# Kernel tuning notes

Measured on AMD Instinct MI355X. Metric: run time of the kernel, lower is better.

Reference implementation:

```python
import jax, jax.numpy as jnp
import numpy as np

EPS = 1e-10
TEMP = 0.01
THETA = 0.1
BETA = 1.0
GAMMA = 1.0  # FocalLoss(gamma=1)
N, C = 32768, 1000


def setup_inputs() -> dict:
    key = jax.random.key(0)
    k1, k2, k3 = jax.random.split(key, 3)
    probs = jax.random.uniform(k1, (N, C), dtype=jnp.float32)
    probs = probs / jnp.sum(probs, axis=1, keepdims=True)  # valid distributions
    lbl = jax.random.randint(k2, (N,), 0, C)
    y = jax.nn.one_hot(lbl, C, dtype=jnp.float32)
    weights = jax.random.uniform(k3, (N, C), dtype=jnp.float32)
    return {"probs": probs, "y": y, "weights": weights}


def _entropy(p):
    return -jnp.sum(p * jnp.log(jnp.clip(p, EPS)), axis=1)


def _soft_T(e):
    num = e * (1.0 - THETA)
    den = jnp.clip((1.0 - e) * THETA, EPS)
    v = (1.0 / TEMP) * jnp.log(jnp.clip(num / den, EPS))
    return jax.nn.sigmoid(v)


def reference(probs, y, weights):
    num_classes = probs.shape[1]
    entmax = jnp.log(jnp.float32(num_classes))

    predictions = jnp.argmax(probs, axis=1)          # [N]
    labels = jnp.argmax(y)                            # scalar (faithful to original)
    unc = _entropy(probs)                             # [N]

    th_list = jnp.linspace(0.0, 1.0, 21, dtype=jnp.float32)
    umin, umax = jnp.min(unc), jnp.max(unc)
    unc_th = umin + th_list * (umax - umin)           # [21]

    acc = (predictions == labels)                     # [N] bool
    s = _soft_T(unc / entmax)                         # [N]
    t = jnp.tanh(unc)                                 # [N]
    cert_w = (1.0 - s) * (1.0 - t)                    # certain weight
    uncw = s * t                                      # uncertain weight

    le = unc[None, :] <= unc_th[:, None]              # [21, N]
    accb = acc[None, :]
    zero = jnp.float32(0.0)
    n_ac = jnp.sum(jnp.where(le & accb, cert_w[None, :], zero), axis=1)
    n_au = jnp.sum(jnp.where((~le) & accb, uncw[None, :], zero), axis=1)
    n_ic = jnp.sum(jnp.where(le & (~accb), cert_w[None, :], zero), axis=1)
    n_iu = jnp.sum(jnp.where((~le) & (~accb), uncw[None, :], zero), axis=1)

    avu = (n_ac + n_iu) / (n_ac + n_au + n_ic + n_iu + EPS)  # [21]
    # trapezoid rule over th_list (increasing -> direction = 1)
    dx = jnp.diff(th_list)
    auc_avu = jnp.sum(0.5 * (avu[1:] + avu[:-1]) * dx)

    logp = jnp.log(jnp.clip(probs, 1e-08))            # FocalLoss eps = 1e-8
    base = y * logp
    focal_loss = jnp.mean(-jnp.sum(base * weights * (1.0 - probs) ** GAMMA, axis=1))
    ce_loss = jnp.mean(-jnp.sum(base, axis=1))

    savu_loss = -BETA * jnp.log(jnp.clip(auc_avu, EPS)) + focal_loss
    return (savu_loss, ce_loss)
```

## Files before the change

kernel.cpp:

```cpp
#include <hip/hip_runtime.h>
#include <hip/hip_bf16.h>

constexpr int kN = 32768;
constexpr int kC = 1000;
constexpr int NB_A = 2048;
constexpr int NB_B = 1024;
constexpr int NB3 = 512;

__global__ __launch_bounds__(256) void k1_main(
    const float* __restrict__ probs, const float* __restrict__ y,
    const float* __restrict__ wts, float* __restrict__ unc,
    int* __restrict__ pred, float* __restrict__ partMM ,
    float* __restrict__ partCF ) {
  const int lane = threadIdx.x & 63;
  const int wid = threadIdx.x >> 6;

  if (blockIdx.x < NB_A) {
    const int gw = blockIdx.x * 4 + wid;
    float mn = 3.4e38f, mx = -3.4e38f;
#pragma unroll 1
    for (int r = 0; r < 4; ++r) {
      const int i = gw + r * 8192;
      const float* pr = probs + (size_t)i * kC;
      float4 p4[4];
#pragma unroll
      for (int k = 0; k < 4; ++k) {
        const int c0 = k * 256 + lane * 4;
        if (c0 < kC) p4[k] = *reinterpret_cast<const float4*>(pr + c0);
        else p4[k] = make_float4(0.f, 0.f, 0.f, 0.f);
      }
      float ent = 0.f, bv = -3.4e38f; int bi = 0;
#pragma unroll
      for (int k = 0; k < 4; ++k) {
        const int c0 = k * 256 + lane * 4;
#pragma unroll
        for (int j = 0; j < 4; ++j) {
          const float p = (&p4[k].x)[j];
          ent += p * logf(fmaxf(p, 1e-10f));
          if (p > bv) { bv = p; bi = c0 + j; }
        }
      }
#pragma unroll
      for (int off = 32; off; off >>= 1) {
        ent += __shfl_xor(ent, off);
        const float bv2 = __shfl_xor(bv, off);
        const int bi2 = __shfl_xor(bi, off);
        if (bv2 > bv || (bv2 == bv && bi2 < bi)) { bv = bv2; bi = bi2; }
      }
      const float u = -ent;
      if (lane == 0) { unc[i] = u; pred[i] = bi; }
      mn = fminf(mn, u); mx = fmaxf(mx, u);
    }
    __shared__ float sMin[4], sMax[4];
    if (lane == 0) { sMin[wid] = mn; sMax[wid] = mx; }
    __syncthreads();
    if (threadIdx.x == 0) {
      float a = 3.4e38f, b = -3.4e38f;
#pragma unroll
      for (int q = 0; q < 4; ++q) { a = fminf(a, sMin[q]); b = fmaxf(b, sMax[q]); }
      partMM[blockIdx.x * 2 + 0] = a;
      partMM[blockIdx.x * 2 + 1] = b;
    }
  } else {
    const int gwb = (blockIdx.x - NB_A) * 4 + wid;
    constexpr float kLogClip8 = -18.420680743952367f;
    float ce = 0.f, fo = 0.f;
#pragma unroll 1
    for (int r = 0; r < 8; ++r) {
      const int i = gwb + r * 4096;
      const float* yr = y + (size_t)i * kC;
      int lbl = -1;
#pragma unroll 1
      for (int step = 0; step < 4; ++step) {
        const int c0 = step * 256 + lane * 4;
        float4 y4 = make_float4(0.f, 0.f, 0.f, 0.f);
        if (c0 < kC) y4 = *reinterpret_cast<const float4*>(yr + c0);
        int loc = -1;
#pragma unroll
        for (int j = 0; j < 4; ++j) if ((&y4.x)[j] != 0.0f) loc = j;
        if (__any(loc >= 0)) {
          if (loc >= 0) lbl = c0 + loc;
          break;
        }
      }
      if (lbl >= 0) {
        const float p = probs[(size_t)i * kC + lbl];
        const float w = wts[(size_t)i * kC + lbl];
        const float lp = fmaxf(logf(fmaxf(p, 1e-10f)), kLogClip8);
        ce += lp;
        fo += lp * w * (1.0f - p);
      }
    }
#pragma unroll
    for (int off = 32; off; off >>= 1) {
      ce += __shfl_xor(ce, off);
      fo += __shfl_xor(fo, off);
    }
    __shared__ float sCe[4], sFo[4];
    if (lane == 0) { sCe[wid] = ce; sFo[wid] = fo; }
    __syncthreads();
    if (threadIdx.x == 0) {
      float c = 0.f, f = 0.f;
#pragma unroll
      for (int q = 0; q < 4; ++q) { c += sCe[q]; f += sFo[q]; }
      const int bb = blockIdx.x - NB_A;
      partCF[bb * 2 + 0] = c;
      partCF[bb * 2 + 1] = f;
    }
  }
}

__global__ __launch_bounds__(256) void k2_scalars(
    const float* __restrict__ y, const float* __restrict__ partMM,
    const float* __restrict__ partCF, float* __restrict__ scal) {
  const int t = threadIdx.x;
  float mn = 3.4e38f, mx = -3.4e38f, c = 0.f, f = 0.f;
  for (int b = t; b < NB_A; b += 256) {
    mn = fminf(mn, partMM[b * 2 + 0]);
    mx = fmaxf(mx, partMM[b * 2 + 1]);
  }
  for (int b = t; b < NB_B; b += 256) {
    c += partCF[b * 2 + 0];
    f += partCF[b * 2 + 1];
  }
  __shared__ float sc[256], sf[256], smn[256], smx[256];
  sc[t] = c; sf[t] = f; smn[t] = mn; smx[t] = mx;
  __syncthreads();
  for (int off = 128; off; off >>= 1) {
    if (t < off) {
      sc[t] += sc[t + off]; sf[t] += sf[t + off];
      smn[t] = fminf(smn[t], smn[t + off]);
      smx[t] = fmaxf(smx[t], smx[t + off]);
    }
    __syncthreads();
  }
  float bv = -3.4e38f; int bi = 0;
  for (int c0 = t; c0 < kC; c0 += 256) {
    const float v = y[c0];
    if (v > bv) { bv = v; bi = c0; }
  }
  __shared__ float sbv[256]; __shared__ int sbi[256];
  sbv[t] = bv; sbi[t] = bi;
  __syncthreads();
  for (int off = 128; off; off >>= 1) {
    if (t < off) {
      if (sbv[t + off] > sbv[t] ||
          (sbv[t + off] == sbv[t] && sbi[t + off] < sbi[t])) {
        sbv[t] = sbv[t + off]; sbi[t] = sbi[t + off];
      }
    }
    __syncthreads();
  }
  if (t == 0) {
    scal[0] = -sc[0] / (float)kN;
    scal[1] = -sf[0] / (float)kN;
    const float umin = smn[0], umax = smx[0];
    scal[2] = umin; scal[3] = umax;
    for (int k = 0; k < 21; ++k) {
      const float th = (float)((double)k * 0.05);
      scal[4 + k] = umin + th * (umax - umin);
    }
    reinterpret_cast<int*>(scal)[25] = sbi[0];
  }
}

__global__ __launch_bounds__(64) void k3_hist(
    const float* __restrict__ unc, const int* __restrict__ pred,
    const float* __restrict__ scal, float* __restrict__ part3 ) {
  __shared__ float hist[88 * 64];
  __shared__ float th[21];
  __shared__ int s_label;
  const int t = threadIdx.x;
  for (int b = 0; b < 88; ++b) hist[b * 64 + t] = 0.f;
  if (t < 21) th[t] = scal[4 + t];
  if (t == 0) s_label = reinterpret_cast<const int*>(scal)[25];
  __syncthreads();
  const float entmax = logf(1000.0f);
  const int label = s_label;

  for (int i = blockIdx.x * 64 + t; i < kN; i += NB3 * 64) {
    const float u = unc[i];
    const bool acc = (pred[i] == label);
    const float e = u / entmax;
    const float num = e * 0.9f;
    const float den = fmaxf((1.0f - e) * 0.1f, 1e-10f);
    const float v = 100.0f * logf(fmaxf(num / den, 1e-10f));
    const float s = 1.0f / (1.0f + expf(-v));
    const float tt = tanhf(u);
    const float cw = (1.0f - s) * (1.0f - tt);
    const float uw = s * tt;
    int k0 = 0;
#pragma unroll
    for (int k = 0; k < 21; ++k) k0 += (th[k] < u) ? 1 : 0;
    const int base = acc ? 0 : 44;
    hist[(base + k0) * 64 + t] += cw;
    hist[(base + 22 + k0) * 64 + t] += uw;
  }
  __syncthreads();
  for (int b = t; b < 88; b += 64) {
    float s2 = 0.f;
    for (int q = 0; q < 64; ++q) s2 += hist[b * 64 + q];
    part3[blockIdx.x * 88 + b] = s2;
  }
}

__global__ __launch_bounds__(128) void k4_final(
    const float* __restrict__ part3, const float* __restrict__ scal,
    float* __restrict__ out) {
  __shared__ float h[88];
  const int t = threadIdx.x;
  for (int b = t; b < 88; b += 128) {
    float s = 0.f;
    for (int q = 0; q < NB3; ++q) s += part3[q * 88 + b];
    h[b] = s;
  }
  __syncthreads();
  if (t == 0) {
    float totAU = 0.f, totIU = 0.f;
    for (int k = 0; k < 22; ++k) { totAU += h[22 + k]; totIU += h[66 + k]; }
    float avu[21];
    float cAC = 0.f, cAU = 0.f, cIC = 0.f, cIU = 0.f;
    for (int k = 0; k < 21; ++k) {
      cAC += h[k]; cAU += h[22 + k]; cIC += h[44 + k]; cIU += h[66 + k];
      const float n_ac = cAC;
      const float n_au = totAU - cAU;
      const float n_ic = cIC;
      const float n_iu = totIU - cIU;
      avu[k] = (n_ac + n_iu) / (n_ac + n_au + n_ic + n_iu + 1e-10f);
    }
    float auc = 0.f;
    for (int k = 0; k < 20; ++k) {
      const float th0 = (float)((double)k * 0.05);
      const float th1 = (float)((double)(k + 1) * 0.05);
      auc += 0.5f * (avu[k + 1] + avu[k]) * (th1 - th0);
    }
    out[0] = -logf(fmaxf(auc, 1e-10f)) + scal[1];
    out[1] = scal[0];
  }
}

extern "C" void kernel_launch(void* const* d_in, const int* in_sizes, int n_in,
                              void* d_out, int out_size, void* d_ws, size_t ws_size,
                              hipStream_t stream) {
  const float* probs = (const float*)d_in[0];
  const float* y     = (const float*)d_in[1];
  const float* wts   = (const float*)d_in[2];
  float* out = (float*)d_out;

  float* ws     = (float*)d_ws;
  float* unc    = ws;
  int*   pred   = (int*)(ws + kN);
  float* partMM = ws + 2 * kN;
  float* partCF = partMM + NB_A * 2;
  float* scal   = partCF + NB_B * 2;
  float* part3  = scal + 32;

  k1_main<<<dim3(NB_A + NB_B), dim3(256), 0, stream>>>(
      probs, y, wts, unc, pred, partMM, partCF);
  k2_scalars<<<dim3(1), dim3(256), 0, stream>>>(y, partMM, partCF, scal);
  k3_hist<<<dim3(NB3), dim3(64), 0, stream>>>(unc, pred, scal, part3);
  k4_final<<<dim3(1), dim3(128), 0, stream>>>(part3, scal, out);
}
```

Measured before the change: 65.91 us.

## Fuse scalar and final reductions via last-block tickets; remap entropy rows to 16-lane groups

The separate single-block scalar and final kernels are folded into the tails of the main and histogram kernels. A last-block atomic ticket, reset by a memset, decides which block does that work, removing two kernel launches and their dependency gaps. The entropy/argmax pass now gives each 16-lane group one row with double-buffered float4 loads, instead of each wave walking four rows serially, which exposes more memory parallelism. Fast __logf replaces logf, with slightly lower accuracy, and the memset adds an extra stream operation.

```diff
diff --git a/kernel.cpp b/kernel.cpp
--- a/kernel.cpp
+++ b/kernel.cpp
@@ -5,59 +5,64 @@
 constexpr int kC = 1000;
 constexpr int NB_A = 2048;
 constexpr int NB_B = 1024;
+constexpr int NB1 = NB_A + NB_B;
 constexpr int NB3 = 512;
 
 __global__ __launch_bounds__(256) void k1_main(
     const float* __restrict__ probs, const float* __restrict__ y,
     const float* __restrict__ wts, float* __restrict__ unc,
     int* __restrict__ pred, float* __restrict__ partMM ,
-    float* __restrict__ partCF ) {
+    float* __restrict__ partCF , float* __restrict__ scal,
+    int* __restrict__ ticket) {
   const int lane = threadIdx.x & 63;
   const int wid = threadIdx.x >> 6;
+  __shared__ float sA[4], sB[4];
+  __shared__ int sLast;
 
   if (blockIdx.x < NB_A) {
-    const int gw = blockIdx.x * 4 + wid;
-    float mn = 3.4e38f, mx = -3.4e38f;
-#pragma unroll 1
-    for (int r = 0; r < 4; ++r) {
-      const int i = gw + r * 8192;
-      const float* pr = probs + (size_t)i * kC;
-      float4 p4[4];
-#pragma unroll
-      for (int k = 0; k < 4; ++k) {
-        const int c0 = k * 256 + lane * 4;
-        if (c0 < kC) p4[k] = *reinterpret_cast<const float4*>(pr + c0);
-        else p4[k] = make_float4(0.f, 0.f, 0.f, 0.f);
-      }
-      float ent = 0.f, bv = -3.4e38f; int bi = 0;
-#pragma unroll
-      for (int k = 0; k < 4; ++k) {
-        const int c0 = k * 256 + lane * 4;
-#pragma unroll
-        for (int j = 0; j < 4; ++j) {
-          const float p = (&p4[k].x)[j];
-          ent += p * logf(fmaxf(p, 1e-10f));
-          if (p > bv) { bv = p; bi = c0 + j; }
-        }
-      }
-#pragma unroll
-      for (int off = 32; off; off >>= 1) {
-        ent += __shfl_xor(ent, off);
-        const float bv2 = __shfl_xor(bv, off);
-        const int bi2 = __shfl_xor(bi, off);
-        if (bv2 > bv || (bv2 == bv && bi2 < bi)) { bv = bv2; bi = bi2; }
-      }
-      const float u = -ent;
-      if (lane == 0) { unc[i] = u; pred[i] = bi; }
-      mn = fminf(mn, u); mx = fmaxf(mx, u);
-    }
-    __shared__ float sMin[4], sMax[4];
-    if (lane == 0) { sMin[wid] = mn; sMax[wid] = mx; }
+    const int sl = lane & 15;
+    const int g = lane >> 4;
+    const int row = blockIdx.x * 16 + wid * 4 + g;
+    const float* pr = probs + (size_t)row * kC;
+
+    float ent = 0.f, bv = -3.4e38f; int bi = 0;
+    float4 buf[2];
+    buf[0] = *reinterpret_cast<const float4*>(pr + sl * 4);
+#pragma unroll
+    for (int s = 0; s < 16; ++s) {
+      if (s + 1 < 16) {
+        const int c0n = (s + 1) * 64 + sl * 4;
+        buf[(s + 1) & 1] = (c0n < kC)
+            ? *reinterpret_cast<const float4*>(pr + c0n)
+            : make_float4(0.f, 0.f, 0.f, 0.f);
+      }
+      const float4 p4 = buf[s & 1];
+      const int c0 = s * 64 + sl * 4;
+#pragma unroll
+      for (int j = 0; j < 4; ++j) {
+        const float p = (&p4.x)[j];
+        ent += p * __logf(fmaxf(p, 1e-10f));
+        if (p > bv) { bv = p; bi = c0 + j; }
+      }
+    }
+#pragma unroll
+    for (int off = 1; off < 16; off <<= 1) {
+      ent += __shfl_xor(ent, off, 16);
+      const float bv2 = __shfl_xor(bv, off, 16);
+      const int bi2 = __shfl_xor(bi, off, 16);
+      if (bv2 > bv || (bv2 == bv && bi2 < bi)) { bv = bv2; bi = bi2; }
+    }
+    const float u = -ent;
+    if (sl == 0) { unc[row] = u; pred[row] = bi; }
+    float mn = u, mx = u;
+    mn = fminf(mn, __shfl_xor(mn, 16)); mx = fmaxf(mx, __shfl_xor(mx, 16));
+    mn = fminf(mn, __shfl_xor(mn, 32)); mx = fmaxf(mx, __shfl_xor(mx, 32));
+    if (lane == 0) { sA[wid] = mn; sB[wid] = mx; }
     __syncthreads();
     if (threadIdx.x == 0) {
       float a = 3.4e38f, b = -3.4e38f;
 #pragma unroll
-      for (int q = 0; q < 4; ++q) { a = fminf(a, sMin[q]); b = fmaxf(b, sMax[q]); }
+      for (int q = 0; q < 4; ++q) { a = fminf(a, sA[q]); b = fmaxf(b, sB[q]); }
       partMM[blockIdx.x * 2 + 0] = a;
       partMM[blockIdx.x * 2 + 1] = b;
     }
@@ -86,7 +91,7 @@
       if (lbl >= 0) {
         const float p = probs[(size_t)i * kC + lbl];
         const float w = wts[(size_t)i * kC + lbl];
-        const float lp = fmaxf(logf(fmaxf(p, 1e-10f)), kLogClip8);
+        const float lp = fmaxf(__logf(fmaxf(p, 1e-10f)), kLogClip8);
         ce += lp;
         fo += lp * w * (1.0f - p);
       }
@@ -96,23 +101,27 @@
       ce += __shfl_xor(ce, off);
       fo += __shfl_xor(fo, off);
     }
-    __shared__ float sCe[4], sFo[4];
-    if (lane == 0) { sCe[wid] = ce; sFo[wid] = fo; }
+    if (lane == 0) { sA[wid] = ce; sB[wid] = fo; }
     __syncthreads();
     if (threadIdx.x == 0) {
       float c = 0.f, f = 0.f;
 #pragma unroll
-      for (int q = 0; q < 4; ++q) { c += sCe[q]; f += sFo[q]; }
+      for (int q = 0; q < 4; ++q) { c += sA[q]; f += sB[q]; }
       const int bb = blockIdx.x - NB_A;
       partCF[bb * 2 + 0] = c;
       partCF[bb * 2 + 1] = f;
     }
   }
-}
-
-__global__ __launch_bounds__(256) void k2_scalars(
-    const float* __restrict__ y, const float* __restrict__ partMM,
-    const float* __restrict__ partCF, float* __restrict__ scal) {
+
+  __syncthreads();
+  if (threadIdx.x == 0) {
+    __threadfence();
+    sLast = (atomicAdd(ticket, 1) == NB1 - 1) ? 1 : 0;
+  }
+  __syncthreads();
+  if (!sLast) return;
+  __threadfence();
+
   const int t = threadIdx.x;
   float mn = 3.4e38f, mx = -3.4e38f, c = 0.f, f = 0.f;
   for (int b = t; b < NB_A; b += 256) {
@@ -166,10 +175,11 @@
 
 __global__ __launch_bounds__(64) void k3_hist(
     const float* __restrict__ unc, const int* __restrict__ pred,
-    const float* __restrict__ scal, float* __restrict__ part3 ) {
+    const float* __restrict__ scal, float* __restrict__ part3 ,
+    float* __restrict__ out, int* __restrict__ ticket) {
   __shared__ float hist[88 * 64];
   __shared__ float th[21];
-  __shared__ int s_label;
+  __shared__ int s_label, sLast;
   const int t = threadIdx.x;
   for (int b = 0; b < 88; ++b) hist[b * 64 + t] = 0.f;
   if (t < 21) th[t] = scal[4 + t];
@@ -202,17 +212,21 @@
     for (int q = 0; q < 64; ++q) s2 += hist[b * 64 + q];
     part3[blockIdx.x * 88 + b] = s2;
   }
-}
-
-__global__ __launch_bounds__(128) void k4_final(
-    const float* __restrict__ part3, const float* __restrict__ scal,
-    float* __restrict__ out) {
+
+  __syncthreads();
+  if (t == 0) {
+    __threadfence();
+    sLast = (atomicAdd(ticket, 1) == NB3 - 1) ? 1 : 0;
+  }
+  __syncthreads();
+  if (!sLast) return;
+  __threadfence();
+
   __shared__ float h[88];
-  const int t = threadIdx.x;
-  for (int b = t; b < 88; b += 128) {
-    float s = 0.f;
-    for (int q = 0; q < NB3; ++q) s += part3[q * 88 + b];
-    h[b] = s;
+  for (int b = t; b < 88; b += 64) {
+    float s2 = 0.f;
+    for (int q = 0; q < NB3; ++q) s2 += part3[q * 88 + b];
+    h[b] = s2;
   }
   __syncthreads();
   if (t == 0) {
@@ -234,7 +248,7 @@
       const float th1 = (float)((double)(k + 1) * 0.05);
       auc += 0.5f * (avu[k + 1] + avu[k]) * (th1 - th0);
     }
-    out[0] = -logf(fmaxf(auc, 1e-10f)) + scal[1];
+    out[0] = -__logf(fmaxf(auc, 1e-10f)) + scal[1];
     out[1] = scal[0];
   }
 }
@@ -254,10 +268,11 @@
   float* partCF = partMM + NB_A * 2;
   float* scal   = partCF + NB_B * 2;
   float* part3  = scal + 32;
-
-  k1_main<<<dim3(NB_A + NB_B), dim3(256), 0, stream>>>(
-      probs, y, wts, unc, pred, partMM, partCF);
-  k2_scalars<<<dim3(1), dim3(256), 0, stream>>>(y, partMM, partCF, scal);
-  k3_hist<<<dim3(NB3), dim3(64), 0, stream>>>(unc, pred, scal, part3);
-  k4_final<<<dim3(1), dim3(128), 0, stream>>>(part3, scal, out);
+  int*   tickets = (int*)(part3 + NB3 * 88);
+
+  hipMemsetAsync(tickets, 0, 2 * sizeof(int), stream);
+  k1_main<<<dim3(NB1), dim3(256), 0, stream>>>(
+      probs, y, wts, unc, pred, partMM, partCF, scal, &tickets[0]);
+  k3_hist<<<dim3(NB3), dim3(64), 0, stream>>>(
+      unc, pred, scal, part3, out, &tickets[1]);
 }
```

New measurement: 174.9 us. 2.65x slower.
